# Optimization experiments

Hardware: AMD Instinct MI355X
Metric: run time of the kernel (lower is better)

## Reference

```python
import jax, jax.numpy as jnp
import numpy as np

WS = 8  # window_size
EPS = 1e-5  # BatchNorm eps


def setup_inputs() -> dict:
    key = jax.random.key(0)
    ks = jax.random.split(key, 11)
    c = 64
    return {
        "x": jax.random.normal(ks[0], (4, c, 256, 256), dtype=jnp.float32),
        "w_in": jax.random.normal(ks[1], (c, c), dtype=jnp.float32) * 0.05,
        "b_in": jax.random.normal(ks[2], (c,), dtype=jnp.float32) * 0.05,
        "bn_gamma": jax.random.uniform(ks[3], (c,), dtype=jnp.float32),
        "bn_beta": jax.random.normal(ks[4], (c,), dtype=jnp.float32) * 0.05,
        "bn_mean": jax.random.normal(ks[5], (c,), dtype=jnp.float32) * 0.05,
        "bn_var": jax.random.uniform(ks[6], (c,), dtype=jnp.float32),
        "w_mask": jax.random.normal(ks[7], (c, c), dtype=jnp.float32) * 0.05,
        "b_mask": jax.random.normal(ks[8], (c,), dtype=jnp.float32) * 0.05,
        "w_out": jax.random.normal(ks[9], (c, c), dtype=jnp.float32) * 0.05,
        "b_out": jax.random.normal(ks[10], (c,), dtype=jnp.float32) * 0.05,
    }


def reference(x, w_in, b_in, bn_gamma, bn_beta, bn_mean, bn_var,
              w_mask, b_mask, w_out, b_out):
    ws = WS
    b, c, h, w = x.shape  # shifts == 0 -> no roll

    # project_inp: 1x1 conv + BatchNorm2d (inference mode, running stats)
    x = jnp.einsum('bchw,oc->bohw', x, w_in) + b_in[None, :, None, None]
    inv = bn_gamma / jnp.sqrt(bn_var + EPS)
    x = (x - bn_mean[None, :, None, None]) * inv[None, :, None, None] \
        + bn_beta[None, :, None, None]

    # seq_refl_win_pad(back=False): pad right/bottom by ws, then copy the
    # preceding ws rows into the bottom pad, then the preceding ws cols
    # (including the new bottom rows) into the right pad.
    x_pad = jnp.concatenate([x, x[:, :, -ws:, :]], axis=2)      # [b,c,h+ws,w]
    x_pad = jnp.concatenate([x_pad, x_pad[:, :, :, -ws:]], axis=3)  # [b,c,h+ws,w+ws]

    hh, ww = h // ws, w // ws
    # mask = Conv2d(kernel=1, stride=2) on the 2ws x 2ws windows ->
    # equivalent to sampling even offsets inside each window, then a 1x1 linear.
    row = (jnp.arange(hh) * ws)[:, None] + jnp.arange(0, 2 * ws, 2)[None, :]  # [hh, ws]
    col = (jnp.arange(ww) * ws)[:, None] + jnp.arange(0, 2 * ws, 2)[None, :]  # [ww, ws]
    g = x_pad[:, :, row, :]        # [b, c, hh, ws_h, w+ws]
    g = g[:, :, :, :, col]         # [b, c, hh, ws_h, ww, ws_w]
    # torch's double unfold yields window dims ordered (W-window, H-window),
    # and q flattens in that (Wwin, Hwin) order -> match exactly.
    g = jnp.transpose(g, (0, 2, 4, 5, 3, 1))        # [b, hh, ww, ws_w, ws_h, c]
    q = g.reshape(b * hh * ww, ws * ws, c)
    q = q @ w_mask.T + b_mask                       # 1x1 conv as per-pixel linear

    # v: non-overlapping ws x ws windows of x, flattened H-major (dh dw)
    v = x.reshape(b, c, hh, ws, ww, ws)
    v = jnp.transpose(v, (0, 2, 4, 3, 5, 1)).reshape(b * hh * ww, ws * ws, c)

    atn = jax.nn.softmax(q @ jnp.swapaxes(q, -1, -2), axis=-1)  # [bn, ws^2, ws^2]
    y = atn @ v                                                  # [bn, ws^2, c]

    # reassemble: '(b h w) (dh dw) c -> b c (h dh) (w dw)'
    y = y.reshape(b, hh, ww, ws, ws, c)
    y = jnp.transpose(y, (0, 5, 1, 3, 2, 4)).reshape(b, c, h, w)

    # project_out: 1x1 conv
    y = jnp.einsum('bchw,oc->bohw', y, w_out) + b_out[None, :, None, None]
    return y
```

## Files before the change

kernel.cpp:

```cpp
#include <hip/hip_runtime.h>

typedef unsigned short ushort_t;
typedef unsigned int uint_t;
typedef __attribute__((ext_vector_type(8))) short short8v;
typedef __attribute__((ext_vector_type(4))) float f32x4;

__device__ __forceinline__ float bf2f(ushort_t u) {
    union { uint_t u; float f; } v; v.u = (uint_t)u << 16; return v.f;
}
__device__ __forceinline__ ushort_t f2bf(float f) {
    union { float f; uint_t u; } v; v.f = f;
    uint_t u = v.u;
    return (ushort_t)((u + 0x7fffu + ((u >> 16) & 1u)) >> 16);
}

#define MFMA(A,B,C) __builtin_amdgcn_mfma_f32_16x16x32_bf16(A, B, C, 0, 0, 0)

__global__ __launch_bounds__(256, 4) void k1_pwbn_mfma(
    const float* __restrict__ x, const float* __restrict__ w_in, const float* __restrict__ b_in,
    const float* __restrict__ gamma, const float* __restrict__ beta,
    const float* __restrict__ mean, const float* __restrict__ var,
    ushort_t* __restrict__ xbn)
{
    __shared__ short xsh[64][72];
    __shared__ short xsl[64][72];
    __shared__ short wfh[64][72];
    __shared__ short wfl[64][72];
    __shared__ float bef[64];

    int tid = threadIdx.x;
    int b   = blockIdx.x >> 10;
    int hw0 = (blockIdx.x & 1023) << 6;
    const float* xb = x + ((size_t)b << 22);

    #pragma unroll
    for (int u = 0; u < 2; ++u) {
        int idx = u * 256 + tid;
        int cp = idx >> 4, pq = idx & 15;
        int c0 = cp * 2, p0 = pq * 4;
        float4 fa = *(const float4*)(xb + (size_t)c0 * 65536 + hw0 + p0);
        float4 fb = *(const float4*)(xb + (size_t)(c0 + 1) * 65536 + hw0 + p0);
        float va[4] = {fa.x, fa.y, fa.z, fa.w};
        float vb[4] = {fb.x, fb.y, fb.z, fb.w};
        #pragma unroll
        for (int e = 0; e < 4; ++e) {
            ushort_t h0 = f2bf(va[e]), h1 = f2bf(vb[e]);
            ushort_t l0 = f2bf(va[e] - bf2f(h0)), l1 = f2bf(vb[e] - bf2f(h1));
            *(uint_t*)&xsh[p0 + e][c0] = (uint_t)h0 | ((uint_t)h1 << 16);
            *(uint_t*)&xsl[p0 + e][c0] = (uint_t)l0 | ((uint_t)l1 << 16);
        }
    }
    #pragma unroll
    for (int v = 0; v < 2; ++v) {
        int idx = v * 256 + tid;
        int o = idx >> 3, c0 = (idx & 7) * 8;
        float sc = gamma[o] * rsqrtf(var[o] + 1e-5f);
        float4 fa = *(const float4*)(w_in + o * 64 + c0);
        float4 fb = *(const float4*)(w_in + o * 64 + c0 + 4);
        float vv[8] = {fa.x, fa.y, fa.z, fa.w, fb.x, fb.y, fb.z, fb.w};
        union { int4 q; ushort_t s[8]; } ph, pl;
        #pragma unroll
        for (int e = 0; e < 8; ++e) {
            float wv = vv[e] * sc;
            ushort_t h = f2bf(wv);
            ph.s[e] = h;
            pl.s[e] = f2bf(wv - bf2f(h));
        }
        *(int4*)&wfh[o][c0] = ph.q;
        *(int4*)&wfl[o][c0] = pl.q;
    }
    if (tid < 64) {
        float inv = gamma[tid] * rsqrtf(var[tid] + 1e-5f);
        bef[tid] = (b_in[tid] - mean[tid]) * inv + beta[tid];
    }
    __syncthreads();

    int w = tid >> 6, l = tid & 63;
    int half = l >> 4, lr = l & 15;
    int k0 = half * 8;

    short8v bh[2], bl[2];
    #pragma unroll
    for (int kc = 0; kc < 2; ++kc) {
        bh[kc] = *(short8v*)&xsh[16 * w + lr][k0 + 32 * kc];
        bl[kc] = *(short8v*)&xsl[16 * w + lr][k0 + 32 * kc];
    }
    short8v ah[4][2], al[4][2];
    #pragma unroll
    for (int ot = 0; ot < 4; ++ot)
        #pragma unroll
        for (int kc = 0; kc < 2; ++kc) {
            ah[ot][kc] = *(short8v*)&wfh[16 * ot + lr][k0 + 32 * kc];
            al[ot][kc] = *(short8v*)&wfl[16 * ot + lr][k0 + 32 * kc];
        }

    ushort_t* xp = xbn + ((size_t)(b * 65536 + hw0 + 16 * w + lr) << 6);
    #pragma unroll
    for (int ot = 0; ot < 4; ++ot) {
        f32x4 acc = {0.f, 0.f, 0.f, 0.f};
        #pragma unroll
        for (int kc = 0; kc < 2; ++kc) {
            acc = MFMA(ah[ot][kc], bh[kc], acc);
            acc = MFMA(ah[ot][kc], bl[kc], acc);
            acc = MFMA(al[ot][kc], bh[kc], acc);
        }
        int o0 = 16 * ot + 4 * half;
        float4 bq = *(const float4*)&bef[o0];
        float bqs[4] = {bq.x, bq.y, bq.z, bq.w};
        ushort_t hs[4];
        #pragma unroll
        for (int rr = 0; rr < 4; ++rr) hs[rr] = f2bf(acc[rr] + bqs[rr]);
        *(uint2*)(xp + o0) = make_uint2((uint_t)hs[0] | ((uint_t)hs[1] << 16),
                                        (uint_t)hs[2] | ((uint_t)hs[3] << 16));
    }
}

#define LDS_G    0
#define LDS_V    9216
#define LDS_WMH  18432
#define LDS_WML  27648
#define LDS_QH   36864
#define LDS_QL   46080
#define LDS_WOH  55296
#define LDS_WOL  64512
#define LDS_RED  73728
#define LDS_RED2 74752
#define LDS_RS   75776
#define LDS_TOT  76032

__device__ __forceinline__ void splitw(const float* src, short* dh, short* dl) {
    union { int4 v; ushort_t s[8]; } h0, h1, l0, l1;
    float4 f0 = *(const float4*)(src);
    float4 f1 = *(const float4*)(src + 4);
    float4 f2 = *(const float4*)(src + 8);
    float4 f3 = *(const float4*)(src + 12);
    float fv[16] = {f0.x,f0.y,f0.z,f0.w, f1.x,f1.y,f1.z,f1.w,
                    f2.x,f2.y,f2.z,f2.w, f3.x,f3.y,f3.z,f3.w};
    #pragma unroll
    for (int e = 0; e < 8; ++e) {
        ushort_t h = f2bf(fv[e]);     h0.s[e] = h; l0.s[e] = f2bf(fv[e] - bf2f(h));
        ushort_t g = f2bf(fv[e + 8]); h1.s[e] = g; l1.s[e] = f2bf(fv[e + 8] - bf2f(g));
    }
    *(int4*)(dh)     = h0.v;
    *(int4*)(dh + 8) = h1.v;
    *(int4*)(dl)     = l0.v;
    *(int4*)(dl + 8) = l1.v;
}

__global__ __launch_bounds__(256, 2) void k2_attn_mfma(
    const ushort_t* __restrict__ xbn,
    const float* __restrict__ w_mask, const float* __restrict__ b_mask,
    const float* __restrict__ w_out,  const float* __restrict__ b_out,
    float* __restrict__ out)
{
    __shared__ char smem[LDS_TOT];
    short* gb   = (short*)(smem + LDS_G);
    short* vb   = (short*)(smem + LDS_V);
    short* wmh  = (short*)(smem + LDS_WMH);
    short* wml  = (short*)(smem + LDS_WML);
    short* qhb  = (short*)(smem + LDS_QH);
    short* qlb  = (short*)(smem + LDS_QL);
    short* woh  = (short*)(smem + LDS_WOH);
    short* wol  = (short*)(smem + LDS_WOL);
    float* Sb   = (float*)(smem + LDS_WMH);
    short* vwt  = (short*)(smem + LDS_G);
    short* pt   = (short*)(smem + LDS_V);
    float* outt = (float*)(smem + LDS_WMH);
    float* red  = (float*)(smem + LDS_RED);
    float* red2 = (float*)(smem + LDS_RED2);
    float* rsv  = (float*)(smem + LDS_RS);

    int tid = threadIdx.x;
    int wid = blockIdx.x;
    int b = wid >> 10, i = (wid >> 5) & 31, j = wid & 31;
    const ushort_t* xb = xbn + ((size_t)b << 22);

    {
        int t = tid >> 2, seg = tid & 3;
        int r = t & 7, s = t >> 3;
        int pr = i * 8 + 2 * r; if (pr >= 256) pr -= 8;
        int pc = j * 8 + 2 * s; if (pc >= 256) pc -= 8;
        const ushort_t* src = xb + (((size_t)((pr << 8) | pc)) << 6) + seg * 16;
        *(int4*)(gb + t * 72 + seg * 16)     = *(const int4*)src;
        *(int4*)(gb + t * 72 + seg * 16 + 8) = *(const int4*)(src + 8);
        int vr = i * 8 + (t >> 3), vc = j * 8 + (t & 7);
        const ushort_t* vsrc = xb + (((size_t)((vr << 8) | vc)) << 6) + seg * 16;
        *(int4*)(vb + t * 72 + seg * 16)     = *(const int4*)vsrc;
        *(int4*)(vb + t * 72 + seg * 16 + 8) = *(const int4*)(vsrc + 8);
        splitw(w_mask + t * 64 + seg * 16, wmh + t * 72 + seg * 16, wml + t * 72 + seg * 16);
    }
    __syncthreads();

    int w = tid >> 6, l = tid & 63;
    int half = l >> 4, lr = l & 15;
    int mrow = (16 * w + lr) * 72;
    int kc0 = half * 8, kc1 = 32 + half * 8;

    {
        int t = tid >> 2, seg = tid & 3;
        splitw(w_out + t * 64 + seg * 16, woh + t * 72 + seg * 16, wol + t * 72 + seg * 16);
    }

    {
        short8v amh0 = *(short8v*)(wmh + mrow + kc0);
        short8v amh1 = *(short8v*)(wmh + mrow + kc1);
        short8v aml0 = *(short8v*)(wml + mrow + kc0);
        short8v aml1 = *(short8v*)(wml + mrow + kc1);
        float4 bm = *(const float4*)(b_mask + 16 * w + half * 4);
        float bmv[4] = {bm.x, bm.y, bm.z, bm.w};
        #pragma unroll
        for (int n = 0; n < 4; ++n) {
            int nrow = (16 * n + lr) * 72;
            short8v bg0 = *(short8v*)(gb + nrow + kc0);
            short8v bg1 = *(short8v*)(gb + nrow + kc1);
            f32x4 acc = {0.f, 0.f, 0.f, 0.f};
            acc = MFMA(amh0, bg0, acc);
            acc = MFMA(amh1, bg1, acc);
            acc = MFMA(aml0, bg0, acc);
            acc = MFMA(aml1, bg1, acc);
            ushort_t hs[4], ls[4];
            #pragma unroll
            for (int rr = 0; rr < 4; ++rr) {
                float qv = acc[rr] + bmv[rr];
                hs[rr] = f2bf(qv);
                ls[rr] = f2bf(qv - bf2f(hs[rr]));
            }
            int qoff = (16 * n + lr) * 72 + 16 * w + half * 4;
            *(uint2*)(qhb + qoff) = make_uint2((uint_t)hs[0] | ((uint_t)hs[1] << 16),
                                               (uint_t)hs[2] | ((uint_t)hs[3] << 16));
            *(uint2*)(qlb + qoff) = make_uint2((uint_t)ls[0] | ((uint_t)ls[1] << 16),
                                               (uint_t)ls[2] | ((uint_t)ls[3] << 16));
        }
    }
    __syncthreads();

    {
        short8v av0 = *(short8v*)(vb + mrow + kc0);
        short8v av1 = *(short8v*)(vb + mrow + kc1);
        #pragma unroll
        for (int n = 0; n < 4; ++n) {
            int nrow = (16 * n + lr) * 72;
            short8v bh0 = *(short8v*)(woh + nrow + kc0);
            short8v bh1 = *(short8v*)(woh + nrow + kc1);
            short8v bl0 = *(short8v*)(wol + nrow + kc0);
            short8v bl1 = *(short8v*)(wol + nrow + kc1);
            f32x4 acc = {0.f, 0.f, 0.f, 0.f};
            acc = MFMA(av0, bh0, acc);
            acc = MFMA(av1, bh1, acc);
            acc = MFMA(av0, bl0, acc);
            acc = MFMA(av1, bl1, acc);
            ushort_t hs[4];
            #pragma unroll
            for (int rr = 0; rr < 4; ++rr) hs[rr] = f2bf(acc[rr]);
            int voff = (16 * n + lr) * 72 + 16 * w + half * 4;
            *(uint2*)(vwt + voff) = make_uint2((uint_t)hs[0] | ((uint_t)hs[1] << 16),
                                               (uint_t)hs[2] | ((uint_t)hs[3] << 16));
        }
    }
    {
        short8v ah0 = *(short8v*)(qhb + mrow + kc0);
        short8v ah1 = *(short8v*)(qhb + mrow + kc1);
        short8v al0 = *(short8v*)(qlb + mrow + kc0);
        short8v al1 = *(short8v*)(qlb + mrow + kc1);
        #pragma unroll
        for (int n = 0; n < 4; ++n) {
            int nrow = (16 * n + lr) * 72;
            short8v bh0 = *(short8v*)(qhb + nrow + kc0);
            short8v bh1 = *(short8v*)(qhb + nrow + kc1);
            short8v bl0 = *(short8v*)(qlb + nrow + kc0);
            short8v bl1 = *(short8v*)(qlb + nrow + kc1);
            f32x4 acc = {0.f, 0.f, 0.f, 0.f};
            acc = MFMA(ah0, bh0, acc);
            acc = MFMA(ah1, bh1, acc);
            acc = MFMA(ah0, bl0, acc);
            acc = MFMA(ah1, bl1, acc);
            acc = MFMA(al0, bh0, acc);
            acc = MFMA(al1, bh1, acc);
            *(f32x4*)(Sb + (16 * n + lr) * 68 + 16 * w + half * 4) = acc;
        }
    }
    __syncthreads();

    {
        int row = tid >> 2, p = tid & 3;
        const float* srow = Sb + row * 68 + p * 16;
        float4 s4[4];
        #pragma unroll
        for (int q = 0; q < 4; ++q) s4[q] = *(const float4*)(srow + 4 * q);
        float m = -1e30f;
        #pragma unroll
        for (int q = 0; q < 4; ++q)
            m = fmaxf(m, fmaxf(fmaxf(s4[q].x, s4[q].y), fmaxf(s4[q].z, s4[q].w)));
        red[row * 4 + p] = m;
        __syncthreads();
        m = fmaxf(fmaxf(red[row * 4 + 0], red[row * 4 + 1]),
                  fmaxf(red[row * 4 + 2], red[row * 4 + 3]));
        union { int4 v; ushort_t s[8]; } pk0, pk1;
        float ssum = 0.f;
        #pragma unroll
        for (int q = 0; q < 4; ++q) {
            float vv[4] = {s4[q].x, s4[q].y, s4[q].z, s4[q].w};
            #pragma unroll
            for (int e = 0; e < 4; ++e) {
                ushort_t h = f2bf(__expf(vv[e] - m));
                ssum += bf2f(h);
                if (q < 2) pk0.s[q * 4 + e] = h; else pk1.s[(q - 2) * 4 + e] = h;
            }
        }
        *(int4*)(pt + row * 72 + p * 16)     = pk0.v;
        *(int4*)(pt + row * 72 + p * 16 + 8) = pk1.v;
        red2[row * 4 + p] = ssum;
        __syncthreads();
        if (p == 0)
            rsv[row] = 1.0f / (red2[row * 4] + red2[row * 4 + 1] +
                               red2[row * 4 + 2] + red2[row * 4 + 3]);
    }
    __syncthreads();

    {
        short8v ap0 = *(short8v*)(pt + mrow + kc0);
        short8v ap1 = *(short8v*)(pt + mrow + kc1);
        float4 rv = *(const float4*)(rsv + 16 * w + half * 4);
        float rvv[4] = {rv.x, rv.y, rv.z, rv.w};
        f32x4 oacc[4];
        #pragma unroll
        for (int n = 0; n < 4; ++n) {
            int nrow = (16 * n + lr) * 72;
            short8v bv0 = *(short8v*)(vwt + nrow + kc0);
            short8v bv1 = *(short8v*)(vwt + nrow + kc1);
            f32x4 acc = {0.f, 0.f, 0.f, 0.f};
            acc = MFMA(ap0, bv0, acc);
            acc = MFMA(ap1, bv1, acc);
            oacc[n] = acc;
        }
        __syncthreads();
        #pragma unroll
        for (int n = 0; n < 4; ++n) {
            float bo = b_out[16 * n + lr];
            float4 wv = make_float4(oacc[n][0] * rvv[0] + bo, oacc[n][1] * rvv[1] + bo,
                                    oacc[n][2] * rvv[2] + bo, oacc[n][3] * rvv[3] + bo);
            *(float4*)(outt + (16 * n + lr) * 68 + 16 * w + half * 4) = wv;
        }
    }
    __syncthreads();

    {
        float* ob = out + ((size_t)b << 22);
        int base = (i * 8) * 256 + j * 8;
        for (int pp = 0; pp < 16; ++pp) {
            int e = pp * 256 + tid;
            int o = e >> 6, t = e & 63;
            ob[((size_t)o << 16) + base + ((t >> 3) << 8) + (t & 7)] = outt[o * 68 + t];
        }
    }
}

extern "C" void kernel_launch(void* const* d_in, const int* in_sizes, int n_in,
                              void* d_out, int out_size, void* d_ws, size_t ws_size,
                              hipStream_t stream) {
    const float* x      = (const float*)d_in[0];
    const float* w_in   = (const float*)d_in[1];
    const float* b_in   = (const float*)d_in[2];
    const float* gamma  = (const float*)d_in[3];
    const float* beta   = (const float*)d_in[4];
    const float* mean   = (const float*)d_in[5];
    const float* var    = (const float*)d_in[6];
    const float* w_mask = (const float*)d_in[7];
    const float* b_mask = (const float*)d_in[8];
    const float* w_out  = (const float*)d_in[9];
    const float* b_out  = (const float*)d_in[10];
    float* out = (float*)d_out;
    ushort_t* xbn = (ushort_t*)d_ws;

    hipLaunchKernelGGL(k1_pwbn_mfma, dim3(4096), dim3(256), 0, stream,
                       x, w_in, b_in, gamma, beta, mean, var, xbn);
    hipLaunchKernelGGL(k2_attn_mfma, dim3(4096), dim3(256), 0, stream,
                       xbn, w_mask, b_mask, w_out, b_out, out);
}
```

Before: 194.7 us.

## Cut attention kernel LDS by splitting weights in registers and shuffle-reducing softmax

```diff
diff --git a/kernel.cpp b/kernel.cpp
--- a/kernel.cpp
+++ b/kernel.cpp
@@ -15,6 +15,18 @@
 }
 
 #define MFMA(A,B,C) __builtin_amdgcn_mfma_f32_16x16x32_bf16(A, B, C, 0, 0, 0)
+
+__device__ __forceinline__ void split8(float4 f0, float4 f1, short8v& h8, short8v& l8) {
+    float v[8] = {f0.x, f0.y, f0.z, f0.w, f1.x, f1.y, f1.z, f1.w};
+    union { short8v v; ushort_t s[8]; } H, L;
+    #pragma unroll
+    for (int e = 0; e < 8; ++e) {
+        ushort_t h = f2bf(v[e]);
+        H.s[e] = h;
+        L.s[e] = f2bf(v[e] - bf2f(h));
+    }
+    h8 = H.v; l8 = L.v;
+}
 
 __global__ __launch_bounds__(256, 4) void k1_pwbn_mfma(
     const float* __restrict__ x, const float* __restrict__ w_in, const float* __restrict__ b_in,
@@ -115,60 +127,30 @@
     }
 }
 
-#define LDS_G    0
-#define LDS_V    9216
-#define LDS_WMH  18432
-#define LDS_WML  27648
-#define LDS_QH   36864
-#define LDS_QL   46080
-#define LDS_WOH  55296
-#define LDS_WOL  64512
-#define LDS_RED  73728
-#define LDS_RED2 74752
-#define LDS_RS   75776
-#define LDS_TOT  76032
-
-__device__ __forceinline__ void splitw(const float* src, short* dh, short* dl) {
-    union { int4 v; ushort_t s[8]; } h0, h1, l0, l1;
-    float4 f0 = *(const float4*)(src);
-    float4 f1 = *(const float4*)(src + 4);
-    float4 f2 = *(const float4*)(src + 8);
-    float4 f3 = *(const float4*)(src + 12);
-    float fv[16] = {f0.x,f0.y,f0.z,f0.w, f1.x,f1.y,f1.z,f1.w,
-                    f2.x,f2.y,f2.z,f2.w, f3.x,f3.y,f3.z,f3.w};
-    #pragma unroll
-    for (int e = 0; e < 8; ++e) {
-        ushort_t h = f2bf(fv[e]);     h0.s[e] = h; l0.s[e] = f2bf(fv[e] - bf2f(h));
-        ushort_t g = f2bf(fv[e + 8]); h1.s[e] = g; l1.s[e] = f2bf(fv[e + 8] - bf2f(g));
-    }
-    *(int4*)(dh)     = h0.v;
-    *(int4*)(dh + 8) = h1.v;
-    *(int4*)(dl)     = l0.v;
-    *(int4*)(dl + 8) = l1.v;
-}
-
-__global__ __launch_bounds__(256, 2) void k2_attn_mfma(
+#define K2_A   0
+#define K2_B   9216
+#define K2_C   18432
+#define K2_D   27648
+#define K2_E   36864
+#define K2_RS  53248
+#define K2_TOT 53504
+
+__global__ __launch_bounds__(256, 3) void k2_attn_v3(
     const ushort_t* __restrict__ xbn,
     const float* __restrict__ w_mask, const float* __restrict__ b_mask,
     const float* __restrict__ w_out,  const float* __restrict__ b_out,
     float* __restrict__ out)
 {
-    __shared__ char smem[LDS_TOT];
-    short* gb   = (short*)(smem + LDS_G);
-    short* vb   = (short*)(smem + LDS_V);
-    short* wmh  = (short*)(smem + LDS_WMH);
-    short* wml  = (short*)(smem + LDS_WML);
-    short* qhb  = (short*)(smem + LDS_QH);
-    short* qlb  = (short*)(smem + LDS_QL);
-    short* woh  = (short*)(smem + LDS_WOH);
-    short* wol  = (short*)(smem + LDS_WOL);
-    float* Sb   = (float*)(smem + LDS_WMH);
-    short* vwt  = (short*)(smem + LDS_G);
-    short* pt   = (short*)(smem + LDS_V);
-    float* outt = (float*)(smem + LDS_WMH);
-    float* red  = (float*)(smem + LDS_RED);
-    float* red2 = (float*)(smem + LDS_RED2);
-    float* rsv  = (float*)(smem + LDS_RS);
+    __shared__ char smem[K2_TOT];
+    short* gb   = (short*)(smem + K2_A);
+    short* vb   = (short*)(smem + K2_B);
+    short* qhb  = (short*)(smem + K2_C);
+    short* qlb  = (short*)(smem + K2_D);
+    float* Sb   = (float*)(smem + K2_E);
+    short* vwt  = (short*)(smem + K2_A);
+    short* pt   = (short*)(smem + K2_B);
+    float* outt = (float*)(smem + K2_E);
+    float* rsv  = (float*)(smem + K2_RS);
 
     int tid = threadIdx.x;
     int wid = blockIdx.x;
@@ -187,7 +169,6 @@
         const ushort_t* vsrc = xb + (((size_t)((vr << 8) | vc)) << 6) + seg * 16;
         *(int4*)(vb + t * 72 + seg * 16)     = *(const int4*)vsrc;
         *(int4*)(vb + t * 72 + seg * 16 + 8) = *(const int4*)(vsrc + 8);
-        splitw(w_mask + t * 64 + seg * 16, wmh + t * 72 + seg * 16, wml + t * 72 + seg * 16);
     }
     __syncthreads();
 
@@ -195,17 +176,13 @@
     int half = l >> 4, lr = l & 15;
     int mrow = (16 * w + lr) * 72;
     int kc0 = half * 8, kc1 = 32 + half * 8;
-
-    {
-        int t = tid >> 2, seg = tid & 3;
-        splitw(w_out + t * 64 + seg * 16, woh + t * 72 + seg * 16, wol + t * 72 + seg * 16);
-    }
-
-    {
-        short8v amh0 = *(short8v*)(wmh + mrow + kc0);
-        short8v amh1 = *(short8v*)(wmh + mrow + kc1);
-        short8v aml0 = *(short8v*)(wml + mrow + kc0);
-        short8v aml1 = *(short8v*)(wml + mrow + kc1);
+    int swz = lr & 7;
+
+    {
+        const float* wmp = w_mask + (16 * w + lr) * 64;
+        short8v amh0, aml0, amh1, aml1;
+        split8(*(const float4*)(wmp + kc0), *(const float4*)(wmp + kc0 + 4), amh0, aml0);
+        split8(*(const float4*)(wmp + kc1), *(const float4*)(wmp + kc1 + 4), amh1, aml1);
         float4 bm = *(const float4*)(b_mask + 16 * w + half * 4);
         float bmv[4] = {bm.x, bm.y, bm.z, bm.w};
         #pragma unroll
@@ -239,11 +216,10 @@
         short8v av1 = *(short8v*)(vb + mrow + kc1);
         #pragma unroll
         for (int n = 0; n < 4; ++n) {
-            int nrow = (16 * n + lr) * 72;
-            short8v bh0 = *(short8v*)(woh + nrow + kc0);
-            short8v bh1 = *(short8v*)(woh + nrow + kc1);
-            short8v bl0 = *(short8v*)(wol + nrow + kc0);
-            short8v bl1 = *(short8v*)(wol + nrow + kc1);
+            const float* wop = w_out + (16 * n + lr) * 64;
+            short8v bh0, bl0, bh1, bl1;
+            split8(*(const float4*)(wop + kc0), *(const float4*)(wop + kc0 + 4), bh0, bl0);
+            split8(*(const float4*)(wop + kc1), *(const float4*)(wop + kc1 + 4), bh1, bl1);
             f32x4 acc = {0.f, 0.f, 0.f, 0.f};
             acc = MFMA(av0, bh0, acc);
             acc = MFMA(av1, bh1, acc);
@@ -276,44 +252,45 @@
             acc = MFMA(ah1, bl1, acc);
             acc = MFMA(al0, bh0, acc);
             acc = MFMA(al1, bh1, acc);
-            *(f32x4*)(Sb + (16 * n + lr) * 68 + 16 * w + half * 4) = acc;
+            int srow = 16 * n + lr;
+            int c4s = (4 * w + half) ^ swz;
+            *(f32x4*)(Sb + srow * 64 + c4s * 4) = acc;
         }
     }
     __syncthreads();
 
     {
         int row = tid >> 2, p = tid & 3;
-        const float* srow = Sb + row * 68 + p * 16;
-        float4 s4[4];
-        #pragma unroll
-        for (int q = 0; q < 4; ++q) s4[q] = *(const float4*)(srow + 4 * q);
+        int rsw = row & 7;
+        const float* srow = Sb + row * 64;
+        f32x4 s4[4];
+        #pragma unroll
+        for (int qq = 0; qq < 4; ++qq)
+            s4[qq] = *(const f32x4*)(srow + (p * 4 + qq) * 4);
         float m = -1e30f;
         #pragma unroll
-        for (int q = 0; q < 4; ++q)
-            m = fmaxf(m, fmaxf(fmaxf(s4[q].x, s4[q].y), fmaxf(s4[q].z, s4[q].w)));
-        red[row * 4 + p] = m;
-        __syncthreads();
-        m = fmaxf(fmaxf(red[row * 4 + 0], red[row * 4 + 1]),
-                  fmaxf(red[row * 4 + 2], red[row * 4 + 3]));
-        union { int4 v; ushort_t s[8]; } pk0, pk1;
+        for (int qq = 0; qq < 4; ++qq)
+            m = fmaxf(m, fmaxf(fmaxf(s4[qq][0], s4[qq][1]), fmaxf(s4[qq][2], s4[qq][3])));
+        m = fmaxf(m, __shfl_xor(m, 1));
+        m = fmaxf(m, __shfl_xor(m, 2));
         float ssum = 0.f;
         #pragma unroll
-        for (int q = 0; q < 4; ++q) {
-            float vv[4] = {s4[q].x, s4[q].y, s4[q].z, s4[q].w};
+        for (int qq = 0; qq < 4; ++qq) {
+            int ucol4 = (p * 4 + qq) ^ rsw;
+            ushort_t hs[4];
             #pragma unroll
             for (int e = 0; e < 4; ++e) {
-                ushort_t h = f2bf(__expf(vv[e] - m));
+                ushort_t h = f2bf(__expf(s4[qq][e] - m));
                 ssum += bf2f(h);
-                if (q < 2) pk0.s[q * 4 + e] = h; else pk1.s[(q - 2) * 4 + e] = h;
+                hs[e] = h;
             }
-        }
-        *(int4*)(pt + row * 72 + p * 16)     = pk0.v;
-        *(int4*)(pt + row * 72 + p * 16 + 8) = pk1.v;
-        red2[row * 4 + p] = ssum;
-        __syncthreads();
-        if (p == 0)
-            rsv[row] = 1.0f / (red2[row * 4] + red2[row * 4 + 1] +
-                               red2[row * 4 + 2] + red2[row * 4 + 3]);
+            *(uint2*)(pt + row * 72 + ucol4 * 4) =
+                make_uint2((uint_t)hs[0] | ((uint_t)hs[1] << 16),
+                           (uint_t)hs[2] | ((uint_t)hs[3] << 16));
+        }
+        ssum += __shfl_xor(ssum, 1);
+        ssum += __shfl_xor(ssum, 2);
+        if (p == 0) rsv[row] = 1.0f / ssum;
     }
     __syncthreads();
 
@@ -322,7 +299,6 @@
         short8v ap1 = *(short8v*)(pt + mrow + kc1);
         float4 rv = *(const float4*)(rsv + 16 * w + half * 4);
         float rvv[4] = {rv.x, rv.y, rv.z, rv.w};
-        f32x4 oacc[4];
         #pragma unroll
         for (int n = 0; n < 4; ++n) {
             int nrow = (16 * n + lr) * 72;
@@ -331,15 +307,12 @@
             f32x4 acc = {0.f, 0.f, 0.f, 0.f};
             acc = MFMA(ap0, bv0, acc);
             acc = MFMA(ap1, bv1, acc);
-            oacc[n] = acc;
-        }
-        __syncthreads();
-        #pragma unroll
-        for (int n = 0; n < 4; ++n) {
-            float bo = b_out[16 * n + lr];
-            float4 wv = make_float4(oacc[n][0] * rvv[0] + bo, oacc[n][1] * rvv[1] + bo,
-                                    oacc[n][2] * rvv[2] + bo, oacc[n][3] * rvv[3] + bo);
-            *(float4*)(outt + (16 * n + lr) * 68 + 16 * w + half * 4) = wv;
+            int orow = 16 * n + lr;
+            float bo = b_out[orow];
+            int c4s = (4 * w + half) ^ swz;
+            f32x4 wv = {acc[0] * rvv[0] + bo, acc[1] * rvv[1] + bo,
+                        acc[2] * rvv[2] + bo, acc[3] * rvv[3] + bo};
+            *(f32x4*)(outt + orow * 64 + c4s * 4) = wv;
         }
     }
     __syncthreads();
@@ -350,7 +323,8 @@
         for (int pp = 0; pp < 16; ++pp) {
             int e = pp * 256 + tid;
             int o = e >> 6, t = e & 63;
-            ob[((size_t)o << 16) + base + ((t >> 3) << 8) + (t & 7)] = outt[o * 68 + t];
+            float val = outt[o * 64 + (((t >> 2) ^ (o & 7)) << 2) + (t & 3)];
+            ob[((size_t)o << 16) + base + ((t >> 3) << 8) + (t & 7)] = val;
         }
     }
 }
@@ -374,6 +348,6 @@
 
     hipLaunchKernelGGL(k1_pwbn_mfma, dim3(4096), dim3(256), 0, stream,
                        x, w_in, b_in, gamma, beta, mean, var, xbn);
-    hipLaunchKernelGGL(k2_attn_mfma, dim3(4096), dim3(256), 0, stream,
+    hipLaunchKernelGGL(k2_attn_v3, dim3(4096), dim3(256), 0, stream,
                        xbn, w_mask, b_mask, w_out, b_out, out);
 }
```

Result: no change. 196.9 us (+1.1%).
